# Optimization experiments

Measured on AMD Instinct MI355X. Metric: run time of the kernel, lower is better.

## Reference

```python
import jax, jax.numpy as jnp
import numpy as np

IN_U = 1024
OUT_U = 1024
BATCH = 4096
HID = 20            # ceil(log2(IN_U*OUT_U)), layer_encoding_dim=0 since num_layers=1
MLP_H = 10
FEAT = 3 + 3 * HID  # 63


def setup_inputs() -> dict:
    key = jax.random.key(0)
    ks = jax.random.split(key, 6)
    X = jax.random.normal(ks[0], (BATCH, IN_U), dtype=jnp.float32)
    weight = jax.random.normal(ks[1], (IN_U, OUT_U), dtype=jnp.float32) * 0.02
    # binary positional encodings per cell (encode_weight_hidden_states)
    k = jnp.arange(IN_U * OUT_U, dtype=jnp.int32).reshape(IN_U, OUT_U)
    shifts = jnp.arange(HID - 1, -1, -1, dtype=jnp.int32)
    hidden = ((k[..., None] >> shifts) & 1).astype(jnp.float32)  # [IN_U, OUT_U, HID]
    W1 = jax.random.normal(ks[2], (FEAT, MLP_H), dtype=jnp.float32) / np.float32(np.sqrt(FEAT))
    b1 = jnp.zeros((MLP_H,), jnp.float32)
    W2 = jax.random.normal(ks[3], (MLP_H, MLP_H), dtype=jnp.float32) / np.float32(np.sqrt(MLP_H))
    b2 = jnp.zeros((MLP_H,), jnp.float32)
    W3 = jax.random.normal(ks[4], (MLP_H, 1 + HID), dtype=jnp.float32) / np.float32(np.sqrt(MLP_H))
    b3 = jnp.zeros((1 + HID,), jnp.float32)
    return {"X": X, "weight": weight, "hidden": hidden,
            "W1": W1, "b1": b1, "W2": W2, "b2": b2, "W3": W3, "b3": b3}


def reference(X, weight, hidden, W1, b1, W2, b2, W3, b3):
    n, m = weight.shape
    # exclude-self column means ('forward') and row means ('backward')
    fwd_mean = (jnp.sum(weight, axis=0, keepdims=True) - weight) / (n - 1)   # [n,m]
    bwd_mean = (jnp.sum(weight, axis=1, keepdims=True) - weight) / (m - 1)   # [n,m]
    fwd_hs = (jnp.sum(hidden, axis=0, keepdims=True) - hidden) / (n - 1)     # [n,m,H]
    bwd_hs = (jnp.sum(hidden, axis=1, keepdims=True) - hidden) / (m - 1)     # [n,m,H]
    feat = jnp.concatenate(
        [weight[..., None], fwd_mean[..., None], bwd_mean[..., None],
         hidden, fwd_hs, bwd_hs], axis=-1)                                   # [n,m,3+3H]
    h = jax.nn.relu(jnp.einsum('nmf,fh->nmh', feat, W1) + b1)
    h = jax.nn.relu(jnp.einsum('nmh,hk->nmk', h, W2) + b2)
    updates = jnp.einsum('nmk,ko->nmo', h, W3) + b3                          # [n,m,1+H]
    new_weight = weight + updates[..., 0]
    # (hidden states also get updates[...,1:] in the torch module, but only the
    #  softmax output is returned)
    logits = jax.nn.relu(X @ new_weight)                                     # [B,m]
    return jax.nn.softmax(logits, axis=-1)
```

## Files before the change

### kernel.cpp

```cpp
#include <hip/hip_runtime.h>
#include <hip/hip_bf16.h>
#include <stdint.h>


#define RS_OFF      0
#define CSPART_OFF  4096
#define BT_OFF      266240
#define AH_OFF      2363392

typedef __attribute__((ext_vector_type(8))) _Float16 f16x8;
typedef __attribute__((ext_vector_type(4))) float f32x4;

__device__ __forceinline__ unsigned short f2h(float x) {
    _Float16 h = (_Float16)x;
    unsigned short u;
    __builtin_memcpy(&u, &h, 2);
    return u;
}
__device__ __forceinline__ void gld16(const void* g, void* l) {
    __builtin_amdgcn_global_load_lds(
        (const __attribute__((address_space(1))) unsigned*)g,
        (__attribute__((address_space(3))) unsigned*)l, 16, 0, 0);
}

__global__ __launch_bounds__(256) void k_pre(const float* __restrict__ w,
        float* __restrict__ rs, float* __restrict__ cs_part) {
    __shared__ float part[4][1024];
    int t = threadIdx.x;
    int lane = t & 63, wv = t >> 6;
    int r0 = blockIdx.x * 16 + wv * 4;
    float ccol[16];
    #pragma unroll
    for (int j = 0; j < 16; ++j) ccol[j] = 0.f;
    #pragma unroll
    for (int rr = 0; rr < 4; ++rr) {
        int row = r0 + rr;
        float rsum = 0.f;
        #pragma unroll
        for (int j = 0; j < 16; ++j) {
            float v = w[(size_t)row * 1024 + j * 64 + lane];
            ccol[j] += v;
            rsum += v;
        }
        #pragma unroll
        for (int o = 32; o; o >>= 1) rsum += __shfl_down(rsum, o);
        if (lane == 0) rs[row] = rsum;
    }
    #pragma unroll
    for (int j = 0; j < 16; ++j) part[wv][j * 64 + lane] = ccol[j];
    __syncthreads();
    #pragma unroll
    for (int j = 0; j < 4; ++j) {
        int c = t + j * 256;
        cs_part[(size_t)blockIdx.x * 1024 + c] =
            part[0][c] + part[1][c] + part[2][c] + part[3][c];
    }
}

__global__ __launch_bounds__(256) void k_nw(const float* __restrict__ w,
        const float* __restrict__ X,
        const float* __restrict__ rs, const float* __restrict__ cs_part,
        const float* __restrict__ W1, const float* __restrict__ b1,
        const float* __restrict__ W2, const float* __restrict__ b2,
        const float* __restrict__ W3, const float* __restrict__ b3,
        unsigned short* __restrict__ Bt, unsigned short* __restrict__ Ah) {
    __shared__ float sW1[630], sW2[100], sb1[10], sb2[10], sw3[10], sa[10];
    __shared__ float rs_loc[32], cs_loc[32];
    __shared__ float rn_loc[320], cm_loc[320];
    __shared__ float st[32][33];
    int t = threadIdx.x;
    if (blockIdx.x >= 1024) {
        int b2x = blockIdx.x - 1024;
        #pragma unroll
        for (int p = 0; p < 4; ++p) {
            size_t idx = (size_t)b2x * 4096 + p * 1024 + t * 4;
            float4 v = *(const float4*)&X[idx];
            ushort4 h;
            h.x = f2h(v.x); h.y = f2h(v.y); h.z = f2h(v.z); h.w = f2h(v.w);
            *(ushort4*)&Ah[idx] = h;
        }
        return;
    }
    int n0 = (blockIdx.x & 31) * 32;
    int m0 = (blockIdx.x >> 5) * 32;
    const float inv = 1.0f / 1023.0f;

    for (int i = t; i < 630; i += 256) sW1[i] = W1[i];
    if (t < 100) sW2[t] = W2[t];
    if (t >= 128 && t < 138) { sb1[t - 128] = b1[t - 128]; sb2[t - 128] = b2[t - 128]; }
    if (t >= 160 && t < 170) sw3[t - 160] = W3[(t - 160) * 21];
    if (t >= 192 && t < 224) rs_loc[t - 192] = rs[n0 + t - 192];
    if (t >= 224 && t < 256) {
        float s = 0.f;
        #pragma unroll
        for (int p = 0; p < 64; ++p) s += cs_part[(size_t)p * 1024 + m0 + (t - 224)];
        cs_loc[t - 224] = s;
    }
    float b30 = b3[0];
    __syncthreads();
    if (t < 10) sa[t] = sW1[t] - (sW1[10 + t] + sW1[20 + t]) * inv;
    for (int id = t; id < 640; id += 256) {
        int h = id % 10, i = (id / 10) & 31, side = id >= 320;
        if (!side) {
            int n = n0 + i;
            float v = rs_loc[i] * sW1[20 + h] * inv;
            #pragma unroll
            for (int j = 0; j < 10; j++) {
                float bit = (float)((n >> (9 - j)) & 1);
                v += bit * (sW1[(3 + j) * 10 + h] + sW1[(43 + j) * 10 + h]
                            - sW1[(23 + j) * 10 + h] * inv);
                v += (512.0f * inv) * sW1[(23 + j) * 10 + h];
            }
            rn_loc[i * 10 + h] = v;
        } else {
            int m = m0 + i;
            float v = cs_loc[i] * sW1[10 + h] * inv + sb1[h];
            #pragma unroll
            for (int j = 0; j < 10; j++) {
                float bit = (float)((m >> (9 - j)) & 1);
                v += bit * (sW1[(13 + j) * 10 + h] + sW1[(33 + j) * 10 + h]
                            - sW1[(53 + j) * 10 + h] * inv);
                v += (512.0f * inv) * sW1[(53 + j) * 10 + h];
            }
            cm_loc[i * 10 + h] = v;
        }
    }
    __syncthreads();
    int ml = t & 31;
    #pragma unroll
    for (int i = 0; i < 4; i++) {
        int nl = (t >> 5) + 8 * i;
        float wv = w[(size_t)(n0 + nl) * 1024 + m0 + ml];
        float h1[10];
        #pragma unroll
        for (int h = 0; h < 10; h++)
            h1[h] = fmaxf(wv * sa[h] + rn_loc[nl * 10 + h] + cm_loc[ml * 10 + h], 0.f);
        float u = b30;
        #pragma unroll
        for (int k = 0; k < 10; k++) {
            float h2 = sb2[k];
            #pragma unroll
            for (int h = 0; h < 10; h++) h2 += h1[h] * sW2[h * 10 + k];
            u += fmaxf(h2, 0.f) * sw3[k];
        }
        st[nl][ml] = wv + u;
    }
    __syncthreads();
    int mrow = t >> 3, kc = t & 7;
    unsigned short hi4[4];
    #pragma unroll
    for (int j = 0; j < 4; j++)
        hi4[j] = f2h(st[kc * 4 + j][mrow]);
    size_t base = (size_t)(m0 + mrow) * 1024 + n0 + kc * 4;
    *(ushort4*)&Bt[base] = make_ushort4(hi4[0], hi4[1], hi4[2], hi4[3]);
}

__global__ __launch_bounds__(256, 2) void k_gemm10(const unsigned short* __restrict__ Ah,
        const unsigned short* __restrict__ Bt, float* __restrict__ out) {
    __shared__ unsigned short sAh[2][128 * 64];
    __shared__ unsigned short sBh[2][64 * 64];
    int tid = threadIdx.x;
    int lane = tid & 63, w = tid >> 6;
    int b = blockIdx.x;
    int xcd = b & 7, s = b >> 3;
    int ty = (xcd << 2) | (s >> 4);
    int tx = s & 15;
    int n0 = tx * 64, m0 = ty * 128;
    int wm = (w >> 1) * 64, wn = (w & 1) * 32;
    int quad = lane >> 4, l16 = lane & 15;

    f32x4 acc[4][2];
    #pragma unroll
    for (int i = 0; i < 4; i++)
        #pragma unroll
        for (int j = 0; j < 2; j++) acc[i][j] = (f32x4)0.f;

#define STAGE_TILE(kb, buf)                                                  \
    do {                                                                     \
        _Pragma("unroll")                                                    \
        for (int s2 = 0; s2 < 4; ++s2) {                                     \
            int P = s2 * 256 + tid;                                          \
            int row = P >> 3;                                                \
            int seg = (P & 7) ^ (row & 7);                                   \
            int ldsOff = (s2 * 256 + w * 64) * 8;      \
            size_t ga = (size_t)(m0 + row) * 1024 + (kb) + seg * 8;          \
            gld16(&Ah[ga], &sAh[buf][ldsOff]);                               \
        }                                                                    \
        _Pragma("unroll")                                                    \
        for (int s2 = 0; s2 < 2; ++s2) {                                     \
            int P = s2 * 256 + tid;                                          \
            int row = P >> 3;                                                \
            int seg = (P & 7) ^ (row & 7);                                   \
            int ldsOff = (s2 * 256 + w * 64) * 8;                            \
            size_t gb = (size_t)(n0 + row) * 1024 + (kb) + seg * 8;          \
            gld16(&Bt[gb], &sBh[buf][ldsOff]);                               \
        }                                                                    \
    } while (0)

    STAGE_TILE(0, 0);
    __syncthreads();

    #pragma unroll 2
    for (int it = 0; it < 16; ++it) {
        int cur = it & 1;
        if (it < 15) STAGE_TILE((it + 1) * 64, cur ^ 1);
        #pragma unroll
        for (int ks = 0; ks < 2; ++ks) {
            int segk = ks * 4 + quad;
            f16x8 ah[4], bh[2];
            #pragma unroll
            for (int i = 0; i < 4; ++i) {
                int ra = wm + i * 16 + l16;
                int ca = (ra * 8 + (segk ^ (ra & 7))) * 8;
                ah[i] = *(const f16x8*)&sAh[cur][ca];
            }
            #pragma unroll
            for (int j = 0; j < 2; ++j) {
                int rb = wn + j * 16 + l16;
                int cb = (rb * 8 + (segk ^ (rb & 7))) * 8;
                bh[j] = *(const f16x8*)&sBh[cur][cb];
            }
            #pragma unroll
            for (int i = 0; i < 4; ++i)
                #pragma unroll
                for (int j = 0; j < 2; ++j)
                    acc[i][j] = __builtin_amdgcn_mfma_f32_16x16x32_f16(ah[i], bh[j], acc[i][j], 0, 0, 0);
        }
        if (it < 15) __syncthreads();
    }
#undef STAGE_TILE

    #pragma unroll
    for (int i = 0; i < 4; ++i) {
        int mr = m0 + wm + i * 16 + quad * 4;
        #pragma unroll
        for (int j = 0; j < 2; ++j) {
            int nc = n0 + wn + j * 16 + l16;
            #pragma unroll
            for (int r = 0; r < 4; ++r)
                out[(size_t)(mr + r) * 1024 + nc] = fmaxf(acc[i][j][r], 0.f);
        }
    }
}

__global__ __launch_bounds__(256) void k_softmax2(float* __restrict__ C) {
    int row = blockIdx.x, t = threadIdx.x, lane = t & 63, wv = t >> 6;
    __shared__ float red[8];
    float4 v = *(float4*)&C[(size_t)row * 1024 + t * 4];
    float lm = fmaxf(fmaxf(v.x, v.y), fmaxf(v.z, v.w));
    #pragma unroll
    for (int o = 32; o; o >>= 1) lm = fmaxf(lm, __shfl_down(lm, o));
    if (lane == 0) red[wv] = lm;
    __syncthreads();
    float mx = fmaxf(fmaxf(red[0], red[1]), fmaxf(red[2], red[3]));
    float4 e;
    e.x = __expf(v.x - mx); e.y = __expf(v.y - mx);
    e.z = __expf(v.z - mx); e.w = __expf(v.w - mx);
    float ls = e.x + e.y + e.z + e.w;
    #pragma unroll
    for (int o = 32; o; o >>= 1) ls += __shfl_down(ls, o);
    if (lane == 0) red[4 + wv] = ls;
    __syncthreads();
    float inv = 1.0f / (red[4] + red[5] + red[6] + red[7]);
    e.x *= inv; e.y *= inv; e.z *= inv; e.w *= inv;
    *(float4*)&C[(size_t)row * 1024 + t * 4] = e;
}

extern "C" void kernel_launch(void* const* d_in, const int* in_sizes, int n_in,
                              void* d_out, int out_size, void* d_ws, size_t ws_size,
                              hipStream_t stream) {
    const float* X  = (const float*)d_in[0];
    const float* W  = (const float*)d_in[1];
    const float* W1 = (const float*)d_in[3];
    const float* b1 = (const float*)d_in[4];
    const float* W2 = (const float*)d_in[5];
    const float* b2 = (const float*)d_in[6];
    const float* W3 = (const float*)d_in[7];
    const float* b3 = (const float*)d_in[8];

    char* wsb = (char*)d_ws;
    float* rs            = (float*)(wsb + RS_OFF);
    float* cs_part       = (float*)(wsb + CSPART_OFF);
    unsigned short* Bt   = (unsigned short*)(wsb + BT_OFF);
    unsigned short* Ah   = (unsigned short*)(wsb + AH_OFF);
    float* out = (float*)d_out;

    k_pre<<<64, 256, 0, stream>>>(W, rs, cs_part);
    k_nw<<<2048, 256, 0, stream>>>(W, X, rs, cs_part, W1, b1, W2, b2, W3, b3, Bt, Ah);
    k_gemm10<<<512, 256, 0, stream>>>(Ah, Bt, out);
    k_softmax2<<<4096, 256, 0, stream>>>(out);
}
```

Before: 178.5 us.

## Fuse softmax into GEMM via cooperative grid sync and remap X conversion rows

After: 317.6 us. 1.78x slower.

```diff
diff --git a/kernel.cpp b/kernel.cpp
--- a/kernel.cpp
+++ b/kernel.cpp
@@ -1,6 +1,9 @@
 #include <hip/hip_runtime.h>
 #include <hip/hip_bf16.h>
+#include <hip/hip_cooperative_groups.h>
 #include <stdint.h>
+
+namespace cg = cooperative_groups;
 
 
 #define RS_OFF      0
@@ -71,9 +74,11 @@
     int t = threadIdx.x;
     if (blockIdx.x >= 1024) {
         int b2x = blockIdx.x - 1024;
+        int rb = (b2x & 7) * 512 + (b2x >> 3) * 4;
+        size_t rbase = (size_t)rb * 1024;
         #pragma unroll
         for (int p = 0; p < 4; ++p) {
-            size_t idx = (size_t)b2x * 4096 + p * 1024 + t * 4;
+            size_t idx = rbase + p * 1024 + t * 4;
             float4 v = *(const float4*)&X[idx];
             ushort4 h;
             h.x = f2h(v.x); h.y = f2h(v.y); h.z = f2h(v.z); h.w = f2h(v.w);
@@ -155,7 +160,7 @@
     *(ushort4*)&Bt[base] = make_ushort4(hi4[0], hi4[1], hi4[2], hi4[3]);
 }
 
-__global__ __launch_bounds__(256, 2) void k_gemm10(const unsigned short* __restrict__ Ah,
+__global__ __launch_bounds__(256, 2) void k_gemm11(const unsigned short* __restrict__ Ah,
         const unsigned short* __restrict__ Bt, float* __restrict__ out) {
     __shared__ unsigned short sAh[2][128 * 64];
     __shared__ unsigned short sBh[2][64 * 64];
@@ -241,29 +246,40 @@
                 out[(size_t)(mr + r) * 1024 + nc] = fmaxf(acc[i][j][r], 0.f);
         }
     }
-}
-
-__global__ __launch_bounds__(256) void k_softmax2(float* __restrict__ C) {
-    int row = blockIdx.x, t = threadIdx.x, lane = t & 63, wv = t >> 6;
-    __shared__ float red[8];
-    float4 v = *(float4*)&C[(size_t)row * 1024 + t * 4];
-    float lm = fmaxf(fmaxf(v.x, v.y), fmaxf(v.z, v.w));
-    #pragma unroll
-    for (int o = 32; o; o >>= 1) lm = fmaxf(lm, __shfl_down(lm, o));
-    if (lane == 0) red[wv] = lm;
-    __syncthreads();
-    float mx = fmaxf(fmaxf(red[0], red[1]), fmaxf(red[2], red[3]));
-    float4 e;
-    e.x = __expf(v.x - mx); e.y = __expf(v.y - mx);
-    e.z = __expf(v.z - mx); e.w = __expf(v.w - mx);
-    float ls = e.x + e.y + e.z + e.w;
-    #pragma unroll
-    for (int o = 32; o; o >>= 1) ls += __shfl_down(ls, o);
-    if (lane == 0) red[4 + wv] = ls;
-    __syncthreads();
-    float inv = 1.0f / (red[4] + red[5] + red[6] + red[7]);
-    e.x *= inv; e.y *= inv; e.z *= inv; e.w *= inv;
-    *(float4*)&C[(size_t)row * 1024 + t * 4] = e;
+
+    __threadfence();
+    cg::this_grid().sync();
+
+    int rbase = xcd * 512 + s * 8 + w * 2;
+    #pragma unroll
+    for (int r = 0; r < 2; ++r) {
+        float* row = out + (size_t)(rbase + r) * 1024;
+        float4 v[4];
+        #pragma unroll
+        for (int j = 0; j < 4; ++j)
+            v[j] = *(float4*)&row[j * 256 + lane * 4];
+        float lm = -1e30f;
+        #pragma unroll
+        for (int j = 0; j < 4; ++j)
+            lm = fmaxf(lm, fmaxf(fmaxf(v[j].x, v[j].y), fmaxf(v[j].z, v[j].w)));
+        #pragma unroll
+        for (int o = 32; o; o >>= 1) lm = fmaxf(lm, __shfl_xor(lm, o));
+        float ls = 0.f;
+        #pragma unroll
+        for (int j = 0; j < 4; ++j) {
+            v[j].x = __expf(v[j].x - lm); v[j].y = __expf(v[j].y - lm);
+            v[j].z = __expf(v[j].z - lm); v[j].w = __expf(v[j].w - lm);
+            ls += v[j].x + v[j].y + v[j].z + v[j].w;
+        }
+        #pragma unroll
+        for (int o = 32; o; o >>= 1) ls += __shfl_xor(ls, o);
+        float inv = 1.0f / ls;
+        #pragma unroll
+        for (int j = 0; j < 4; ++j) {
+            v[j].x *= inv; v[j].y *= inv; v[j].z *= inv; v[j].w *= inv;
+            *(float4*)&row[j * 256 + lane * 4] = v[j];
+        }
+    }
 }
 
 extern "C" void kernel_launch(void* const* d_in, const int* in_sizes, int n_in,
@@ -287,6 +303,12 @@
 
     k_pre<<<64, 256, 0, stream>>>(W, rs, cs_part);
     k_nw<<<2048, 256, 0, stream>>>(W, X, rs, cs_part, W1, b1, W2, b2, W3, b3, Bt, Ah);
-    k_gemm10<<<512, 256, 0, stream>>>(Ah, Bt, out);
-    k_softmax2<<<4096, 256, 0, stream>>>(out);
-}
+    {
+        const unsigned short* aAh = Ah;
+        const unsigned short* aBt = Bt;
+        float* aOut = out;
+        void* args[] = { (void*)&aAh, (void*)&aBt, (void*)&aOut };
+        hipLaunchCooperativeKernel((const void*)k_gemm11, dim3(512), dim3(256),
+                                   args, 0, stream);
+    }
+}
```
